# Optimization experiments

Hardware: AMD Instinct MI355X
Metric: run time of the kernel (lower is better)

Reference implementation:

```python
import jax, jax.numpy as jnp
import numpy as np
from jax import lax

LMBDA = 10.0
MAX_ITERATIONS = 100
MAX_DISTANCE = 5.0
B_, M_, N_ = 8, 1024, 1024


def sinkhorn(M, lmbda=LMBDA, max_iterations=MAX_ITERATIONS, max_distance=MAX_DISTANCE):
    # K = exp(-lmbda * clamp_max(M, max_distance)); uniform marginals r=1/m, c=1/n
    b, m, n = M.shape
    K = jnp.exp(-lmbda * jnp.minimum(M, max_distance))          # (b, m, n)
    KT = jnp.swapaxes(K, -2, -1)                                # (b, n, m)
    r = jnp.full((b, m, 1), 1.0 / m, dtype=M.dtype)
    c = jnp.full((b, n, 1), 1.0 / n, dtype=M.dtype)
    # Fixed-count Sinkhorn iterations (original breaks early on convergence;
    # running the full count reaches the same fixed point).
    def body(u, _):
        u = r / (K @ (c / (KT @ u)))
        return u, None
    u, _ = lax.scan(body, r, None, length=max_iterations)
    v = c / (KT @ u)                                            # (b, n, 1)
    P = u * K * jnp.swapaxes(v, -2, -1)                         # (b, m, n)
    return P


def setup_inputs() -> dict:
    key = jax.random.key(0)
    M = jax.random.uniform(key, (B_, M_, N_), dtype=jnp.float32)  # non-negative costs
    return {"M": M}


def reference(M):
    return sinkhorn(M)
```

## Files before the change

### kernel.cpp

```cpp
#include <hip/hip_runtime.h>
#include <math.h>


#define B_    8
#define N_    1024
#define G_    32
#define RPB   32
#define KSTR  1028
#define NITER 100
#define TPB   256
#define LMB   10.0f
#define MAXD  5.0f

#define LDS_FLOATS (RPB * KSTR + N_ + RPB + 4 * G_)

typedef unsigned long long u64;

__device__ __forceinline__ void st8(float* p, float a, float b) {
    float2 f2 = make_float2(a, b);
    __hip_atomic_store((u64*)p, __builtin_bit_cast(u64, f2),
                       __ATOMIC_RELAXED, __HIP_MEMORY_SCOPE_AGENT);
}
__device__ __forceinline__ float2 ld8(const float* p) {
    u64 raw = __hip_atomic_load((const u64*)p,
                                __ATOMIC_RELAXED, __HIP_MEMORY_SCOPE_AGENT);
    return __builtin_bit_cast(float2, raw);
}
__device__ __forceinline__ void publish(int* s, int v) {
    __atomic_signal_fence(__ATOMIC_SEQ_CST);
    __hip_atomic_store(s, v, __ATOMIC_RELAXED, __HIP_MEMORY_SCOPE_AGENT);
}
__device__ __forceinline__ void poll32(const int* st, int tgt) {
    const int l = threadIdx.x & 31;
    for (;;) {
        int s = __hip_atomic_load(&st[l], __ATOMIC_RELAXED,
                                  __HIP_MEMORY_SCOPE_AGENT);
        if (__all(s >= tgt)) break;
        __builtin_amdgcn_s_sleep(2);
    }
    __atomic_signal_fence(__ATOMIC_SEQ_CST);
}

__global__ void __launch_bounds__(TPB, 1)
sinkhorn_kernel(const float* __restrict__ Mg,
                float* __restrict__ Pg,
                float* __restrict__ part,
                float* __restrict__ vbuf,
                int* __restrict__ stA,
                int* __restrict__ stV)
{
    extern __shared__ float lds[];
    float* Kl   = lds;
    float* vl   = lds + RPB * KSTR;
    float* ul   = vl + N_;
    float4* red = (float4*)(ul + RPB);

    const int b    = blockIdx.x & (B_ - 1);
    const int g    = blockIdx.x >> 3;
    const int t    = threadIdx.x;
    const int row0 = g * RPB;
    const float r = 1.0f / (float)N_;
    const float c = 1.0f / (float)N_;

    const float* Mb = Mg + ((size_t)b * N_ + row0) * N_;
    for (int i = 0; i < RPB; ++i) {
        float4 m4 = ((const float4*)(Mb + (size_t)i * N_))[t];
        float4 k4;
        k4.x = expf(-LMB * fminf(m4.x, MAXD));
        k4.y = expf(-LMB * fminf(m4.y, MAXD));
        k4.z = expf(-LMB * fminf(m4.z, MAXD));
        k4.w = expf(-LMB * fminf(m4.w, MAXD));
        *(float4*)&Kl[i * KSTR + 4 * t] = k4;
    }
    if (t < RPB) ul[t] = r;
    __syncthreads();

    for (int it = 0; it <= NITER; ++it) {
        const int p   = it & 1;
        const int tgt = it + 1;
        int* stA_pb = stA + ((size_t)p * B_ + b) * G_;
        int* stV_pb = stV + ((size_t)p * B_ + b) * G_;

        float4 a = make_float4(0.f, 0.f, 0.f, 0.f);
#pragma unroll
        for (int i = 0; i < RPB; ++i) {
            const float u  = ul[i];
            const float4 k4 = *(const float4*)&Kl[i * KSTR + 4 * t];
            a.x = fmaf(k4.x, u, a.x);
            a.y = fmaf(k4.y, u, a.y);
            a.z = fmaf(k4.z, u, a.z);
            a.w = fmaf(k4.w, u, a.w);
        }
        float* slot = part + (((size_t)p * B_ + b) * G_ + g) * N_;
        st8(&slot[4 * t],     a.x, a.y);
        st8(&slot[4 * t + 2], a.z, a.w);

        __syncthreads();
        if (t == 0) publish(&stA_pb[g], tgt);

        poll32(stA_pb, tgt);
        {
            const int gp = t >> 3;
            const int q  = t & 7;
            const float* pb = part + (((size_t)p * B_ + b) * G_ + gp) * N_
                            + 32 * g + 4 * q;
            float2 s0 = ld8(pb);
            float2 s1 = ld8(pb + 2);
            float4 acc = make_float4(s0.x, s0.y, s1.x, s1.y);
#pragma unroll
            for (int d = 8; d <= 32; d <<= 1) {
                acc.x += __shfl_xor(acc.x, d);
                acc.y += __shfl_xor(acc.y, d);
                acc.z += __shfl_xor(acc.z, d);
                acc.w += __shfl_xor(acc.w, d);
            }
            const int wv = t >> 6;
            if ((t & 63) < 8) red[wv * 8 + (t & 63)] = acc;
        }
        __syncthreads();
        float* vb = vbuf + ((size_t)p * B_ + b) * N_;
        if (t < 8) {
            float4 y4;
            y4.x = red[t].x + red[8 + t].x + red[16 + t].x + red[24 + t].x;
            y4.y = red[t].y + red[8 + t].y + red[16 + t].y + red[24 + t].y;
            y4.z = red[t].z + red[8 + t].z + red[16 + t].z + red[24 + t].z;
            y4.w = red[t].w + red[8 + t].w + red[16 + t].w + red[24 + t].w;
            st8(&vb[32 * g + 4 * t],     c / y4.x, c / y4.y);
            st8(&vb[32 * g + 4 * t + 2], c / y4.z, c / y4.w);
        }
        if (t == 0) {
            __atomic_signal_fence(__ATOMIC_SEQ_CST);
            __builtin_amdgcn_s_waitcnt(0);
            publish(&stV_pb[g], tgt);
        }

        poll32(stV_pb, tgt);
        {
            float2 w0 = ld8(&vb[4 * t]);
            float2 w1 = ld8(&vb[4 * t + 2]);
            *(float4*)&vl[4 * t] = make_float4(w0.x, w0.y, w1.x, w1.y);
        }
        __syncthreads();

        if (it == NITER) break;

        const int rI = t >> 3;
        const int l  = t & 7;
        float4 za = make_float4(0.f, 0.f, 0.f, 0.f);
#pragma unroll
        for (int k2 = 0; k2 < 32; ++k2) {
            const int j0 = 4 * l + 32 * k2;
            const float4 k4 = *(const float4*)&Kl[rI * KSTR + j0];
            const float4 vv = *(const float4*)&vl[j0];
            za.x = fmaf(k4.x, vv.x, za.x);
            za.y = fmaf(k4.y, vv.y, za.y);
            za.z = fmaf(k4.z, vv.z, za.z);
            za.w = fmaf(k4.w, vv.w, za.w);
        }
        float z = za.x + za.y + za.z + za.w;
        z += __shfl_xor(z, 1);
        z += __shfl_xor(z, 2);
        z += __shfl_xor(z, 4);
        if (l == 0) ul[rI] = r / z;
        __syncthreads();
    }

    float* Pb = Pg + ((size_t)b * N_ + row0) * N_;
    const float4 v4 = *(const float4*)&vl[4 * t];
    for (int i = 0; i < RPB; ++i) {
        const float u  = ul[i];
        const float4 k4 = *(const float4*)&Kl[i * KSTR + 4 * t];
        float4 p4;
        p4.x = u * k4.x * v4.x;
        p4.y = u * k4.y * v4.y;
        p4.z = u * k4.z * v4.z;
        p4.w = u * k4.w * v4.w;
        ((float4*)(Pb + (size_t)i * N_))[t] = p4;
    }
}

extern "C" void kernel_launch(void* const* d_in, const int* in_sizes, int n_in,
                              void* d_out, int out_size, void* d_ws, size_t ws_size,
                              hipStream_t stream) {
    const float* M = (const float*)d_in[0];
    float* P = (float*)d_out;

    const size_t part_floats = (size_t)2 * B_ * G_ * N_;
    const size_t v_floats    = (size_t)2 * B_ * N_;
    float* part = (float*)d_ws;
    float* vbuf = part + part_floats;
    int*   stA  = (int*)(vbuf + v_floats);
    int*   stV  = stA + 2 * B_ * G_;
    (void)hipMemsetAsync(stA, 0, (size_t)4 * B_ * G_ * sizeof(int), stream);

    const size_t lds_bytes = (size_t)LDS_FLOATS * sizeof(float);
    (void)hipFuncSetAttribute((const void*)sinkhorn_kernel,
                              hipFuncAttributeMaxDynamicSharedMemorySize,
                              (int)lds_bytes);

    void* args[] = { (void*)&M, (void*)&P, (void*)&part, (void*)&vbuf,
                     (void*)&stA, (void*)&stV };
    hipError_t e = hipLaunchCooperativeKernel((void*)sinkhorn_kernel,
                                              dim3(B_ * G_), dim3(TPB),
                                              args, (unsigned)lds_bytes, stream);
    if (e != hipSuccess) {
        sinkhorn_kernel<<<dim3(B_ * G_), dim3(TPB), lds_bytes, stream>>>(
            M, P, part, vbuf, stA, stV);
    }
}
```

Baseline: 610.2 us.

## Use per-wave readiness flags and targeted polling to drop block barrier

Each wavefront now publishes its own readiness flag for the partial-sum phase, replacing the block-wide barrier followed by a single-thread publish. Each wave then polls only the flags of the producer waves whose partial data it actually reads. The goal is to shorten the critical path of the inter-block handshake in each iteration. It also adds a spin-count timeout with an LDS 'dead' flag that breaks out of polling. That timeout could let the kernel silently produce wrong results instead of hanging, and it adds a check to every poll loop.

```diff
diff --git a/kernel.cpp b/kernel.cpp
--- a/kernel.cpp
+++ b/kernel.cpp
@@ -12,7 +12,7 @@
 #define LMB   10.0f
 #define MAXD  5.0f
 
-#define LDS_FLOATS (RPB * KSTR + N_ + RPB + 4 * G_)
+#define LDS_FLOATS (RPB * KSTR + N_ + RPB + 4 * G_ + 4)
 
 typedef unsigned long long u64;
 
@@ -30,12 +30,14 @@
     __atomic_signal_fence(__ATOMIC_SEQ_CST);
     __hip_atomic_store(s, v, __ATOMIC_RELAXED, __HIP_MEMORY_SCOPE_AGENT);
 }
-__device__ __forceinline__ void poll32(const int* st, int tgt) {
-    const int l = threadIdx.x & 31;
+__device__ __forceinline__ void poll_idx(const int* st, int idx, int tgt,
+                                         int* dead) {
+    int spin = 0;
     for (;;) {
-        int s = __hip_atomic_load(&st[l], __ATOMIC_RELAXED,
+        int s = __hip_atomic_load(&st[idx], __ATOMIC_RELAXED,
                                   __HIP_MEMORY_SCOPE_AGENT);
         if (__all(s >= tgt)) break;
+        if (dead[0] || ++spin > (1 << 18)) { dead[0] = 1; break; }
         __builtin_amdgcn_s_sleep(2);
     }
     __atomic_signal_fence(__ATOMIC_SEQ_CST);
@@ -54,13 +56,17 @@
     float* vl   = lds + RPB * KSTR;
     float* ul   = vl + N_;
     float4* red = (float4*)(ul + RPB);
+    int*   ctl  = (int*)(red + G_);
 
     const int b    = blockIdx.x & (B_ - 1);
     const int g    = blockIdx.x >> 3;
     const int t    = threadIdx.x;
+    const int wv   = t >> 6;
+    const int lane = t & 63;
     const int row0 = g * RPB;
     const float r = 1.0f / (float)N_;
     const float c = 1.0f / (float)N_;
+    int* dead = ctl;
 
     const float* Mb = Mg + ((size_t)b * N_ + row0) * N_;
     for (int i = 0; i < RPB; ++i) {
@@ -73,12 +79,13 @@
         *(float4*)&Kl[i * KSTR + 4 * t] = k4;
     }
     if (t < RPB) ul[t] = r;
+    if (t == 0) ctl[0] = 0;
     __syncthreads();
 
     for (int it = 0; it <= NITER; ++it) {
         const int p   = it & 1;
         const int tgt = it + 1;
-        int* stA_pb = stA + ((size_t)p * B_ + b) * G_;
+        int* stA_pb = stA + ((size_t)p * B_ + b) * (G_ * 4);
         int* stV_pb = stV + ((size_t)p * B_ + b) * G_;
 
         float4 a = make_float4(0.f, 0.f, 0.f, 0.f);
@@ -95,10 +102,11 @@
         st8(&slot[4 * t],     a.x, a.y);
         st8(&slot[4 * t + 2], a.z, a.w);
 
-        __syncthreads();
-        if (t == 0) publish(&stA_pb[g], tgt);
-
-        poll32(stA_pb, tgt);
+        __atomic_signal_fence(__ATOMIC_SEQ_CST);
+        __builtin_amdgcn_s_waitcnt(0);
+        if (lane == 0) publish(&stA_pb[g * 4 + wv], tgt);
+
+        poll_idx(stA_pb, (8 * wv + (lane & 7)) * 4 + (g >> 3), tgt, dead);
         {
             const int gp = t >> 3;
             const int q  = t & 7;
@@ -114,8 +122,7 @@
                 acc.z += __shfl_xor(acc.z, d);
                 acc.w += __shfl_xor(acc.w, d);
             }
-            const int wv = t >> 6;
-            if ((t & 63) < 8) red[wv * 8 + (t & 63)] = acc;
+            if (lane < 8) red[wv * 8 + lane] = acc;
         }
         __syncthreads();
         float* vb = vbuf + ((size_t)p * B_ + b) * N_;
@@ -134,7 +141,7 @@
             publish(&stV_pb[g], tgt);
         }
 
-        poll32(stV_pb, tgt);
+        poll_idx(stV_pb, 8 * wv + (lane & 7), tgt, dead);
         {
             float2 w0 = ld8(&vb[4 * t]);
             float2 w1 = ld8(&vb[4 * t + 2]);
@@ -190,8 +197,9 @@
     float* part = (float*)d_ws;
     float* vbuf = part + part_floats;
     int*   stA  = (int*)(vbuf + v_floats);
-    int*   stV  = stA + 2 * B_ * G_;
-    (void)hipMemsetAsync(stA, 0, (size_t)4 * B_ * G_ * sizeof(int), stream);
+    int*   stV  = stA + 2 * B_ * G_ * 4;
+    (void)hipMemsetAsync(stA, 0, (size_t)(2 * B_ * G_ * 4 + 2 * B_ * G_)
+                         * sizeof(int), stream);
 
     const size_t lds_bytes = (size_t)LDS_FLOATS * sizeof(float);
     (void)hipFuncSetAttribute((const void*)sinkhorn_kernel,
```

Result: slower. 1.199 ms (+96.6%).

## Replace flag-based inter-block sync with tagged value packets

Applied to the files above, without the earlier changes.

Each partial sum and v value is now stored as a 64-bit packet carrying the iteration tag next to the float. Consumers spin on the data itself until the tags match, which drops the separate status-flag publish/poll round trips, the extra barriers and the double buffering. The costs are twice the global traffic for partials and per-element polling. A spin-count fallback with a shared dead flag was added, so a stalled producer could let stale data through silently. A large workspace memset now runs on every launch.

```diff
diff --git a/kernel.cpp b/kernel.cpp
--- a/kernel.cpp
+++ b/kernel.cpp
@@ -12,48 +12,56 @@
 #define LMB   10.0f
 #define MAXD  5.0f
 
-#define LDS_FLOATS (RPB * KSTR + N_ + RPB + 4 * G_)
+#define LDS_FLOATS (RPB * KSTR + N_ + RPB + 4 * G_ + 4)
 
 typedef unsigned long long u64;
 
-__device__ __forceinline__ void st8(float* p, float a, float b) {
-    float2 f2 = make_float2(a, b);
-    __hip_atomic_store((u64*)p, __builtin_bit_cast(u64, f2),
-                       __ATOMIC_RELAXED, __HIP_MEMORY_SCOPE_AGENT);
-}
-__device__ __forceinline__ float2 ld8(const float* p) {
-    u64 raw = __hip_atomic_load((const u64*)p,
-                                __ATOMIC_RELAXED, __HIP_MEMORY_SCOPE_AGENT);
-    return __builtin_bit_cast(float2, raw);
-}
-__device__ __forceinline__ void publish(int* s, int v) {
-    __atomic_signal_fence(__ATOMIC_SEQ_CST);
-    __hip_atomic_store(s, v, __ATOMIC_RELAXED, __HIP_MEMORY_SCOPE_AGENT);
-}
-__device__ __forceinline__ void poll32(const int* st, int tgt) {
-    const int l = threadIdx.x & 31;
+__device__ __forceinline__ void stp(u64* p, float d, int tag) {
+    u64 raw = ((u64)(unsigned)tag << 32) | (u64)__float_as_uint(d);
+    __hip_atomic_store(p, raw, __ATOMIC_RELAXED, __HIP_MEMORY_SCOPE_AGENT);
+}
+__device__ __forceinline__ int dead_ld(int* dead) {
+    return __hip_atomic_load(dead, __ATOMIC_RELAXED,
+                             __HIP_MEMORY_SCOPE_WORKGROUP);
+}
+__device__ __forceinline__ void dead_st(int* dead) {
+    __hip_atomic_store(dead, 1, __ATOMIC_RELAXED,
+                       __HIP_MEMORY_SCOPE_WORKGROUP);
+}
+__device__ __forceinline__ float4 ldp4(const u64* p, int tag, int* dead) {
+    u64 r0, r1, r2, r3;
+    int spin = 0;
     for (;;) {
-        int s = __hip_atomic_load(&st[l], __ATOMIC_RELAXED,
-                                  __HIP_MEMORY_SCOPE_AGENT);
-        if (__all(s >= tgt)) break;
-        __builtin_amdgcn_s_sleep(2);
-    }
-    __atomic_signal_fence(__ATOMIC_SEQ_CST);
+        r0 = __hip_atomic_load(p + 0, __ATOMIC_RELAXED,
+                               __HIP_MEMORY_SCOPE_AGENT);
+        r1 = __hip_atomic_load(p + 1, __ATOMIC_RELAXED,
+                               __HIP_MEMORY_SCOPE_AGENT);
+        r2 = __hip_atomic_load(p + 2, __ATOMIC_RELAXED,
+                               __HIP_MEMORY_SCOPE_AGENT);
+        r3 = __hip_atomic_load(p + 3, __ATOMIC_RELAXED,
+                               __HIP_MEMORY_SCOPE_AGENT);
+        if (((int)(r0 >> 32) == tag) && ((int)(r1 >> 32) == tag) &&
+            ((int)(r2 >> 32) == tag) && ((int)(r3 >> 32) == tag)) break;
+        if (++spin > (1 << 18) || dead_ld(dead)) { dead_st(dead); break; }
+    }
+    return make_float4(__uint_as_float((unsigned)r0),
+                       __uint_as_float((unsigned)r1),
+                       __uint_as_float((unsigned)r2),
+                       __uint_as_float((unsigned)r3));
 }
 
 __global__ void __launch_bounds__(TPB, 1)
 sinkhorn_kernel(const float* __restrict__ Mg,
                 float* __restrict__ Pg,
-                float* __restrict__ part,
-                float* __restrict__ vbuf,
-                int* __restrict__ stA,
-                int* __restrict__ stV)
+                u64* __restrict__ partT,
+                u64* __restrict__ vT)
 {
     extern __shared__ float lds[];
     float* Kl   = lds;
     float* vl   = lds + RPB * KSTR;
     float* ul   = vl + N_;
     float4* red = (float4*)(ul + RPB);
+    int*   ctl  = (int*)(red + G_);
 
     const int b    = blockIdx.x & (B_ - 1);
     const int g    = blockIdx.x >> 3;
@@ -61,6 +69,10 @@
     const int row0 = g * RPB;
     const float r = 1.0f / (float)N_;
     const float c = 1.0f / (float)N_;
+    int* dead = ctl;
+
+    u64* partb = partT + ((size_t)b * G_ + g) * N_;
+    u64* vb    = vT + (size_t)b * N_;
 
     const float* Mb = Mg + ((size_t)b * N_ + row0) * N_;
     for (int i = 0; i < RPB; ++i) {
@@ -73,13 +85,12 @@
         *(float4*)&Kl[i * KSTR + 4 * t] = k4;
     }
     if (t < RPB) ul[t] = r;
+    if (t == 0) ctl[0] = 0;
     __syncthreads();
 
     for (int it = 0; it <= NITER; ++it) {
-        const int p   = it & 1;
-        const int tgt = it + 1;
-        int* stA_pb = stA + ((size_t)p * B_ + b) * G_;
-        int* stV_pb = stV + ((size_t)p * B_ + b) * G_;
+        const int tgtA = it + 1;
+        const int tgtV = (1 << 30) + it + 1;
 
         float4 a = make_float4(0.f, 0.f, 0.f, 0.f);
 #pragma unroll
@@ -91,22 +102,17 @@
             a.z = fmaf(k4.z, u, a.z);
             a.w = fmaf(k4.w, u, a.w);
         }
-        float* slot = part + (((size_t)p * B_ + b) * G_ + g) * N_;
-        st8(&slot[4 * t],     a.x, a.y);
-        st8(&slot[4 * t + 2], a.z, a.w);
-
-        __syncthreads();
-        if (t == 0) publish(&stA_pb[g], tgt);
-
-        poll32(stA_pb, tgt);
+        stp(&partb[4 * t + 0], a.x, tgtA);
+        stp(&partb[4 * t + 1], a.y, tgtA);
+        stp(&partb[4 * t + 2], a.z, tgtA);
+        stp(&partb[4 * t + 3], a.w, tgtA);
+
         {
             const int gp = t >> 3;
             const int q  = t & 7;
-            const float* pb = part + (((size_t)p * B_ + b) * G_ + gp) * N_
-                            + 32 * g + 4 * q;
-            float2 s0 = ld8(pb);
-            float2 s1 = ld8(pb + 2);
-            float4 acc = make_float4(s0.x, s0.y, s1.x, s1.y);
+            const u64* pb = partT + ((size_t)b * G_ + gp) * N_
+                          + 32 * g + 4 * q;
+            float4 acc = ldp4(pb, tgtA, dead);
 #pragma unroll
             for (int d = 8; d <= 32; d <<= 1) {
                 acc.x += __shfl_xor(acc.x, d);
@@ -118,27 +124,21 @@
             if ((t & 63) < 8) red[wv * 8 + (t & 63)] = acc;
         }
         __syncthreads();
-        float* vb = vbuf + ((size_t)p * B_ + b) * N_;
         if (t < 8) {
             float4 y4;
             y4.x = red[t].x + red[8 + t].x + red[16 + t].x + red[24 + t].x;
             y4.y = red[t].y + red[8 + t].y + red[16 + t].y + red[24 + t].y;
             y4.z = red[t].z + red[8 + t].z + red[16 + t].z + red[24 + t].z;
             y4.w = red[t].w + red[8 + t].w + red[16 + t].w + red[24 + t].w;
-            st8(&vb[32 * g + 4 * t],     c / y4.x, c / y4.y);
-            st8(&vb[32 * g + 4 * t + 2], c / y4.z, c / y4.w);
-        }
-        if (t == 0) {
-            __atomic_signal_fence(__ATOMIC_SEQ_CST);
-            __builtin_amdgcn_s_waitcnt(0);
-            publish(&stV_pb[g], tgt);
-        }
-
-        poll32(stV_pb, tgt);
+            stp(&vb[32 * g + 4 * t + 0], c / y4.x, tgtV);
+            stp(&vb[32 * g + 4 * t + 1], c / y4.y, tgtV);
+            stp(&vb[32 * g + 4 * t + 2], c / y4.z, tgtV);
+            stp(&vb[32 * g + 4 * t + 3], c / y4.w, tgtV);
+        }
+
         {
-            float2 w0 = ld8(&vb[4 * t]);
-            float2 w1 = ld8(&vb[4 * t + 2]);
-            *(float4*)&vl[4 * t] = make_float4(w0.x, w0.y, w1.x, w1.y);
+            float4 w = ldp4(&vb[4 * t], tgtV, dead);
+            *(float4*)&vl[4 * t] = w;
         }
         __syncthreads();
 
@@ -185,26 +185,24 @@
     const float* M = (const float*)d_in[0];
     float* P = (float*)d_out;
 
-    const size_t part_floats = (size_t)2 * B_ * G_ * N_;
-    const size_t v_floats    = (size_t)2 * B_ * N_;
-    float* part = (float*)d_ws;
-    float* vbuf = part + part_floats;
-    int*   stA  = (int*)(vbuf + v_floats);
-    int*   stV  = stA + 2 * B_ * G_;
-    (void)hipMemsetAsync(stA, 0, (size_t)4 * B_ * G_ * sizeof(int), stream);
+    const size_t part_pkts = (size_t)B_ * G_ * N_;
+    const size_t v_pkts    = (size_t)B_ * N_;
+    u64* partT = (u64*)d_ws;
+    u64* vT    = partT + part_pkts;
+    (void)hipMemsetAsync(partT, 0, (part_pkts + v_pkts) * sizeof(u64),
+                         stream);
 
     const size_t lds_bytes = (size_t)LDS_FLOATS * sizeof(float);
     (void)hipFuncSetAttribute((const void*)sinkhorn_kernel,
                               hipFuncAttributeMaxDynamicSharedMemorySize,
                               (int)lds_bytes);
 
-    void* args[] = { (void*)&M, (void*)&P, (void*)&part, (void*)&vbuf,
-                     (void*)&stA, (void*)&stV };
+    void* args[] = { (void*)&M, (void*)&P, (void*)&partT, (void*)&vT };
     hipError_t e = hipLaunchCooperativeKernel((void*)sinkhorn_kernel,
                                               dim3(B_ * G_), dim3(TPB),
                                               args, (unsigned)lds_bytes, stream);
     if (e != hipSuccess) {
         sinkhorn_kernel<<<dim3(B_ * G_), dim3(TPB), lds_bytes, stream>>>(
-            M, P, part, vbuf, stA, stV);
-    }
-}
+            M, P, partT, vT);
+    }
+}
```

Result: slower. 1.431 ms (+134.5%).
